# Kernel optimization log

Measured on AMD Instinct MI355X. Metric: run time of the kernel, lower is better.

Reference implementation:

```python
import jax, jax.numpy as jnp
import numpy as np

NEG_SLOPE = 0.2


def gat_conv(x, src, dst, W, a_src, a_dst, b, heads, out_ch, concat):
    """PyG-style GATConv (eval mode, self-loops already appended to src/dst)."""
    N = x.shape[0]
    h = (x @ W).reshape(N, heads, out_ch)            # [N,H,C]
    alpha_s = jnp.einsum('nhc,hc->nh', h, a_src)     # [N,H]
    alpha_d = jnp.einsum('nhc,hc->nh', h, a_dst)
    e = jax.nn.leaky_relu(alpha_s[src] + alpha_d[dst], NEG_SLOPE)  # [E,H]
    # segment softmax over incoming edges per destination node
    m = jax.ops.segment_max(e, dst, num_segments=N)  # every node has a self loop
    ex = jnp.exp(e - m[dst])
    denom = jax.ops.segment_sum(ex, dst, num_segments=N)
    alpha = ex / (denom[dst] + 1e-16)                # [E,H]
    msg = h[src] * alpha[:, :, None]                 # [E,H,C]
    out = jax.ops.segment_sum(msg, dst, num_segments=N)  # [N,H,C]
    if concat:
        out = out.reshape(N, heads * out_ch)
    else:
        out = out.mean(axis=1)
    return out + b


def setup_inputs() -> dict:
    key = jax.random.key(0)
    ks = jax.random.split(key, 12)
    N, E, F_IN = 100000, 3200000, 512
    H1, C1 = 8, 8           # conv1: heads=8, out=8, concat -> 64
    H2, C2 = 8, 16          # conv2: heads=8, out=num_classes=16, mean over heads
    x = jax.random.normal(ks[0], (N, F_IN), dtype=jnp.float32)
    edge_index = jax.random.randint(ks[1], (2, E), 0, N, dtype=jnp.int32)
    g = lambda k, s, fan: jax.random.normal(k, s, dtype=jnp.float32) / np.sqrt(fan)
    return {
        'x': x,
        'edge_index': edge_index,
        'W1': g(ks[2], (F_IN, H1 * C1), F_IN),
        'a_src1': g(ks[3], (H1, C1), C1),
        'a_dst1': g(ks[4], (H1, C1), C1),
        'b1': jnp.zeros((H1 * C1,), jnp.float32),
        'W2': g(ks[5], (H1 * C1, H2 * C2), H1 * C1),
        'a_src2': g(ks[6], (H2, C2), C2),
        'a_dst2': g(ks[7], (H2, C2), C2),
        'b2': jnp.zeros((C2,), jnp.float32),
    }


def reference(x, edge_index, W1, a_src1, a_dst1, b1, W2, a_src2, a_dst2, b2):
    N = x.shape[0]
    loops = jnp.arange(N, dtype=edge_index.dtype)
    src = jnp.concatenate([edge_index[0], loops])
    dst = jnp.concatenate([edge_index[1], loops])
    h = gat_conv(x, src, dst, W1, a_src1, a_dst1, b1, heads=8, out_ch=8, concat=True)
    h = jax.nn.elu(h)
    out = gat_conv(h, src, dst, W2, a_src2, a_dst2, b2, heads=8, out_ch=16, concat=False)
    return out
```

## Files before the change

kernel.cpp:

```cpp
#include <hip/hip_runtime.h>
#include <hip/hip_bf16.h>
#include <hip/hip_fp16.h>
#include <cstddef>

#define NEG_SLOPE 0.2f


__global__ __launch_bounds__(256) void bucket_hist_k(const int* __restrict__ dst, int E,
                                                     int* __restrict__ bhist, int NB) {
    __shared__ int lh[256];
    for (int t = threadIdx.x; t < 256; t += 256) lh[t] = 0;
    __syncthreads();
    int per = (E + gridDim.x - 1) / gridDim.x;
    int s = blockIdx.x * per;
    int e = min(s + per, E);
    for (int i = s + threadIdx.x; i < e; i += 256) atomicAdd(&lh[dst[i] >> 9], 1);
    __syncthreads();
    for (int t = threadIdx.x; t < NB; t += 256)
        if (lh[t]) atomicAdd(&bhist[t], lh[t]);
}

__global__ __launch_bounds__(256) void bucket_scan_k(const int* __restrict__ bhist, int NB,
                                                     int* __restrict__ bbase, int* __restrict__ cursor,
                                                     int* __restrict__ row_start, int N, int E) {
    __shared__ int tmp[256];
    int tid = threadIdx.x;
    int v = (tid < NB) ? bhist[tid] : 0;
    tmp[tid] = v;
    __syncthreads();
    for (int d = 1; d < 256; d <<= 1) {
        int t = tmp[tid];
        int a = (tid >= d) ? tmp[tid - d] : 0;
        __syncthreads();
        tmp[tid] = t + a;
        __syncthreads();
    }
    if (tid < NB) {
        int b = tmp[tid] - v;
        bbase[tid] = b;
        cursor[tid] = b;
    }
    if (tid == 0) {
        bbase[NB] = E;
        row_start[N] = E;
    }
}

__global__ __launch_bounds__(256) void partition_k(const int* __restrict__ src,
                                                   const int* __restrict__ dst, int E,
                                                   int* __restrict__ cursor,
                                                   unsigned int* __restrict__ part, int NB) {
    __shared__ int lh[256];
    __shared__ int lbase[256];
    for (int t = threadIdx.x; t < 256; t += 256) lh[t] = 0;
    __syncthreads();
    int per = (E + gridDim.x - 1) / gridDim.x;
    int s = blockIdx.x * per;
    int e = min(s + per, E);
    for (int i = s + threadIdx.x; i < e; i += 256) atomicAdd(&lh[dst[i] >> 9], 1);
    __syncthreads();
    for (int t = threadIdx.x; t < NB; t += 256) {
        int c = lh[t];
        lbase[t] = c ? atomicAdd(&cursor[t], c) : 0;
        lh[t] = 0;
    }
    __syncthreads();
    for (int i = s + threadIdx.x; i < e; i += 256) {
        int d = dst[i];
        int b = d >> 9;
        int lo = atomicAdd(&lh[b], 1);
        part[lbase[b] + lo] = ((unsigned)src[i] << 9) | (unsigned)(d & 511);
    }
}

__global__ __launch_bounds__(512) void bucket_build_k(const unsigned int* __restrict__ part,
                                                      const int* __restrict__ bbase,
                                                      int* __restrict__ row_start,
                                                      int* __restrict__ csr, int N) {
    __shared__ int cnt[512];
    __shared__ int cur[512];
    int b = blockIdx.x, tid = threadIdx.x;
    int n0 = b << 9;
    int s = bbase[b], e2 = bbase[b + 1];
    cnt[tid] = 0;
    __syncthreads();
    for (int i = s + tid; i < e2; i += 512) atomicAdd(&cnt[part[i] & 511], 1);
    __syncthreads();
    int v = cnt[tid];
    for (int d = 1; d < 512; d <<= 1) {
        int t = cnt[tid];
        int a = (tid >= d) ? cnt[tid - d] : 0;
        __syncthreads();
        cnt[tid] = t + a;
        __syncthreads();
    }
    int excl = cnt[tid] - v;
    if (n0 + tid < N) row_start[n0 + tid] = s + excl;
    cur[tid] = excl;
    __syncthreads();
    for (int i = s + tid; i < e2; i += 512) {
        unsigned u = part[i];
        int p = atomicAdd(&cur[u & 511], 1);
        csr[s + p] = (int)(u >> 9);
    }
}


#define BM 64
#define BN 64
#define BKT 32

__global__ __launch_bounds__(256) void sgemm_k(const float* __restrict__ A,
                                               const float* __restrict__ B,
                                               __half* __restrict__ C,
                                               int M, int Nc, int K) {
    __shared__ __align__(16) float As[BKT][BM + 4];
    __shared__ __align__(16) float Bs[BKT][BN];
    int bm = blockIdx.x * BM;
    int bn = blockIdx.y * BN;
    int t = threadIdx.x;
    int tc = t & 15;
    int tr = t >> 4;
    float acc[4][4] = {};

    for (int k0 = 0; k0 < K; k0 += BKT) {
        {
            int row = t >> 3;
            int kk = (t & 7) << 2;
#pragma unroll
            for (int p = 0; p < 2; ++p) {
                int r = row + p * 32;
                int gr = bm + r;
                float4 v = make_float4(0.f, 0.f, 0.f, 0.f);
                if (gr < M) v = *(const float4*)(A + (size_t)gr * K + k0 + kk);
                As[kk + 0][r] = v.x; As[kk + 1][r] = v.y;
                As[kk + 2][r] = v.z; As[kk + 3][r] = v.w;
            }
        }
        {
            int bk = t >> 4;
            int cc = (t & 15) << 2;
#pragma unroll
            for (int p = 0; p < 2; ++p) {
                int k = bk + p * 16;
                *(float4*)(&Bs[k][cc]) = *(const float4*)(B + (size_t)(k0 + k) * Nc + bn + cc);
            }
        }
        __syncthreads();
#pragma unroll
        for (int kk2 = 0; kk2 < BKT; ++kk2) {
            float4 a4 = *(const float4*)(&As[kk2][tr << 2]);
            float4 b4 = *(const float4*)(&Bs[kk2][tc << 2]);
            float av[4] = {a4.x, a4.y, a4.z, a4.w};
            float bv[4] = {b4.x, b4.y, b4.z, b4.w};
#pragma unroll
            for (int i = 0; i < 4; ++i)
#pragma unroll
                for (int j = 0; j < 4; ++j)
                    acc[i][j] = fmaf(av[i], bv[j], acc[i][j]);
        }
        __syncthreads();
    }
#pragma unroll
    for (int i = 0; i < 4; ++i) {
        int gr = bm + (tr << 2) + i;
        if (gr < M) {
            ushort4 p;
            p.x = __half_as_ushort(__float2half(acc[i][0]));
            p.y = __half_as_ushort(__float2half(acc[i][1]));
            p.z = __half_as_ushort(__float2half(acc[i][2]));
            p.w = __half_as_ushort(__float2half(acc[i][3]));
            *(ushort4*)(C + (size_t)gr * Nc + bn + (tc << 2)) = p;
        }
    }
}


template <int C>
__global__ void alpha_k(const __half* __restrict__ h, const float* __restrict__ a_s,
                        const float* __restrict__ a_d, float* __restrict__ os,
                        float* __restrict__ od, int NH) {
    int i = blockIdx.x * 256 + threadIdx.x;
    if (i >= NH) return;
    int hh = i & 7;
    const __half* hp = h + (size_t)i * C;
    float s = 0.f, d = 0.f;
#pragma unroll
    for (int c = 0; c < C; ++c) {
        float v = __half2float(hp[c]);
        s = fmaf(v, a_s[hh * C + c], s);
        d = fmaf(v, a_d[hh * C + c], d);
    }
    os[i] = s;
    od[i] = d;
}


__global__ __launch_bounds__(64) void aggregate1_k(
    const __half* __restrict__ h1, const float* __restrict__ as,
    const float* __restrict__ ad, const int* __restrict__ row_start,
    const int* __restrict__ csr, const float* __restrict__ b1,
    float* __restrict__ h1o, int N) {
    int n = blockIdx.x;
    int l = threadIdx.x;
    int h = l >> 3;
    int j = l & 7;
    int lbase = l & 56;
    float adv = ad[n * 8 + h];
    float e0 = as[n * 8 + h] + adv;
    e0 = fmaxf(e0, NEG_SLOPE * e0);
    float ex0 = __expf(e0);
    float denom = ex0;
    float acc = ex0 * __half2float(h1[(size_t)n * 64 + l]);
    int e = row_start[n], end = row_start[n + 1];
    int batched = e + ((end - e) & ~7);
    for (; e < batched; e += 8) {
        int sj = csr[e + j];
        float aj = as[sj * 8 + h];
        float t = aj + adv;
        t = fmaxf(t, NEG_SLOPE * t);
        float xj = __expf(t);
#pragma unroll
        for (int q = 0; q < 8; ++q) {
            int sq = __shfl(sj, q, 64);
            float xq = __shfl(xj, lbase + q, 64);
            float v = __half2float(h1[(size_t)sq * 64 + l]);
            denom += xq;
            acc = fmaf(xq, v, acc);
        }
    }
    for (; e < end; ++e) {
        int s0 = csr[e];
        float t = as[s0 * 8 + h] + adv;
        t = fmaxf(t, NEG_SLOPE * t);
        float x0 = __expf(t);
        denom += x0;
        acc = fmaf(x0, __half2float(h1[(size_t)s0 * 64 + l]), acc);
    }
    float v = acc / denom + b1[l];
    h1o[(size_t)n * 64 + l] = v > 0.f ? v : expm1f(v);
}


__global__ __launch_bounds__(64) void aggregate2_k(
    const __half* __restrict__ h2, const float* __restrict__ as,
    const float* __restrict__ ad, const int* __restrict__ row_start,
    const int* __restrict__ csr, const float* __restrict__ b2,
    float* __restrict__ out, int N) {
    int n = blockIdx.x;
    int l = threadIdx.x;
    int h = l >> 3;
    int j = l & 7;
    int lbase = l & 56;
    const __half2* H = (const __half2*)h2;
    float adv = ad[n * 8 + h];
    float e0 = as[n * 8 + h] + adv;
    e0 = fmaxf(e0, NEG_SLOPE * e0);
    float ex0 = __expf(e0);
    float denom = ex0;
    float2 self = __half22float2(H[(size_t)n * 64 + l]);
    float accx = ex0 * self.x, accy = ex0 * self.y;
    int e = row_start[n], end = row_start[n + 1];
    int batched = e + ((end - e) & ~7);
    for (; e < batched; e += 8) {
        int sj = csr[e + j];
        float aj = as[sj * 8 + h];
        float t = aj + adv;
        t = fmaxf(t, NEG_SLOPE * t);
        float xj = __expf(t);
#pragma unroll
        for (int q = 0; q < 8; ++q) {
            int sq = __shfl(sj, q, 64);
            float xq = __shfl(xj, lbase + q, 64);
            float2 v = __half22float2(H[(size_t)sq * 64 + l]);
            denom += xq;
            accx = fmaf(xq, v.x, accx);
            accy = fmaf(xq, v.y, accy);
        }
    }
    for (; e < end; ++e) {
        int s0 = csr[e];
        float t = as[s0 * 8 + h] + adv;
        t = fmaxf(t, NEG_SLOPE * t);
        float x0 = __expf(t);
        float2 v = __half22float2(H[(size_t)s0 * 64 + l]);
        denom += x0;
        accx = fmaf(x0, v.x, accx);
        accy = fmaf(x0, v.y, accy);
    }
    float rx = accx / denom, ry = accy / denom;
#pragma unroll
    for (int m = 8; m <= 32; m <<= 1) {
        rx += __shfl_xor(rx, m, 64);
        ry += __shfl_xor(ry, m, 64);
    }
    if (l < 8) {
        int c0 = l * 2;
        float2 o;
        o.x = rx * 0.125f + b2[c0];
        o.y = ry * 0.125f + b2[c0 + 1];
        *(float2*)(out + (size_t)n * 16 + c0) = o;
    }
}


extern "C" void kernel_launch(void* const* d_in, const int* in_sizes, int n_in,
                              void* d_out, int out_size, void* d_ws, size_t ws_size,
                              hipStream_t stream) {
    (void)n_in; (void)out_size; (void)ws_size;
    const float* x      = (const float*)d_in[0];
    const int*   ei     = (const int*)d_in[1];
    const float* W1     = (const float*)d_in[2];
    const float* a_src1 = (const float*)d_in[3];
    const float* a_dst1 = (const float*)d_in[4];
    const float* b1     = (const float*)d_in[5];
    const float* W2     = (const float*)d_in[6];
    const float* a_src2 = (const float*)d_in[7];
    const float* a_dst2 = (const float*)d_in[8];
    const float* b2     = (const float*)d_in[9];

    int N = in_sizes[0] / 512;
    int E = in_sizes[1] / 2;
    const int* src = ei;
    const int* dst = ei + E;
    int NB = (N + 511) >> 9;

    char* ws = (char*)d_ws;
    size_t off = 0;
    auto alloc = [&](size_t bytes) -> void* {
        void* p = ws + off;
        off = (off + bytes + 255) & ~(size_t)255;
        return p;
    };
    __half* h1  = (__half*)alloc((size_t)N * 64 * 2);
    float*  h1o = (float*)alloc((size_t)N * 64 * 4);
    __half* h2  = (__half*)alloc((size_t)N * 128 * 2);
    float* as1  = (float*)alloc((size_t)N * 8 * 4);
    float* ad1  = (float*)alloc((size_t)N * 8 * 4);
    float* as2  = (float*)alloc((size_t)N * 8 * 4);
    float* ad2  = (float*)alloc((size_t)N * 8 * 4);
    int* row_start = (int*)alloc((size_t)(N + 1) * 4);
    int* bhist     = (int*)alloc(256 * 4);
    int* bbase     = (int*)alloc(257 * 4);
    int* cursor    = (int*)alloc(256 * 4);
    unsigned int* part = (unsigned int*)alloc((size_t)E * 4);
    int* csr       = (int*)alloc((size_t)E * 4);

    hipMemsetAsync(bhist, 0, 256 * 4, stream);
    bucket_hist_k<<<512, 256, 0, stream>>>(dst, E, bhist, NB);
    bucket_scan_k<<<1, 256, 0, stream>>>(bhist, NB, bbase, cursor, row_start, N, E);
    partition_k<<<512, 256, 0, stream>>>(src, dst, E, cursor, part, NB);
    bucket_build_k<<<NB, 512, 0, stream>>>(part, bbase, row_start, csr, N);

    dim3 g1((N + BM - 1) / BM, 1);
    sgemm_k<<<g1, 256, 0, stream>>>(x, W1, h1, N, 64, 512);
    alpha_k<8><<<(N * 8 + 255) / 256, 256, 0, stream>>>(h1, a_src1, a_dst1, as1, ad1, N * 8);
    aggregate1_k<<<N, 64, 0, stream>>>(h1, as1, ad1, row_start, csr, b1, h1o, N);

    dim3 g2((N + BM - 1) / BM, 2);
    sgemm_k<<<g2, 256, 0, stream>>>(h1o, W2, h2, N, 128, 64);
    alpha_k<16><<<(N * 8 + 255) / 256, 256, 0, stream>>>(h2, a_src2, a_dst2, as2, ad2, N * 8);
    aggregate2_k<<<N, 64, 0, stream>>>(h2, as2, ad2, row_start, csr, b2, (float*)d_out, N);
}
```

Before: 714.8 us.

## Replace FP32 SIMT GEMMs with FP16 MFMA GEMMs and store h1o as half

Swaps the shared-memory FP32 SGEMM for a matrix-core kernel using 16x16x32 FP16 MFMA. The weights are converted to a transposed FP16 layout by a small kernel on every call, and the x activations are cast to FP16 on the fly. The first aggregate now writes its output in half precision, which halves the traffic into the second GEMM. The cost being targeted is FP32 ALU-bound GEMM time, mainly x@W1 with K=512. In exchange it loses precision on inputs and intermediates, and operands are loaded straight from global memory without LDS staging.

```diff
diff --git a/kernel.cpp b/kernel.cpp
--- a/kernel.cpp
+++ b/kernel.cpp
@@ -4,6 +4,9 @@
 #include <cstddef>
 
 #define NEG_SLOPE 0.2f
+
+typedef _Float16 half8 __attribute__((ext_vector_type(8)));
+typedef float floatx4 __attribute__((ext_vector_type(4)));
 
 
 __global__ __launch_bounds__(256) void bucket_hist_k(const int* __restrict__ dst, int E,
@@ -106,73 +109,53 @@
 }
 
 
-#define BM 64
-#define BN 64
-#define BKT 32
-
-__global__ __launch_bounds__(256) void sgemm_k(const float* __restrict__ A,
-                                               const float* __restrict__ B,
-                                               __half* __restrict__ C,
-                                               int M, int Nc, int K) {
-    __shared__ __align__(16) float As[BKT][BM + 4];
-    __shared__ __align__(16) float Bs[BKT][BN];
-    int bm = blockIdx.x * BM;
-    int bn = blockIdx.y * BN;
-    int t = threadIdx.x;
-    int tc = t & 15;
-    int tr = t >> 4;
-    float acc[4][4] = {};
-
-    for (int k0 = 0; k0 < K; k0 += BKT) {
-        {
-            int row = t >> 3;
-            int kk = (t & 7) << 2;
-#pragma unroll
-            for (int p = 0; p < 2; ++p) {
-                int r = row + p * 32;
-                int gr = bm + r;
-                float4 v = make_float4(0.f, 0.f, 0.f, 0.f);
-                if (gr < M) v = *(const float4*)(A + (size_t)gr * K + k0 + kk);
-                As[kk + 0][r] = v.x; As[kk + 1][r] = v.y;
-                As[kk + 2][r] = v.z; As[kk + 3][r] = v.w;
-            }
-        }
-        {
-            int bk = t >> 4;
-            int cc = (t & 15) << 2;
-#pragma unroll
-            for (int p = 0; p < 2; ++p) {
-                int k = bk + p * 16;
-                *(float4*)(&Bs[k][cc]) = *(const float4*)(B + (size_t)(k0 + k) * Nc + bn + cc);
-            }
-        }
-        __syncthreads();
-#pragma unroll
-        for (int kk2 = 0; kk2 < BKT; ++kk2) {
-            float4 a4 = *(const float4*)(&As[kk2][tr << 2]);
-            float4 b4 = *(const float4*)(&Bs[kk2][tc << 2]);
-            float av[4] = {a4.x, a4.y, a4.z, a4.w};
-            float bv[4] = {b4.x, b4.y, b4.z, b4.w};
-#pragma unroll
-            for (int i = 0; i < 4; ++i)
-#pragma unroll
-                for (int j = 0; j < 4; ++j)
-                    acc[i][j] = fmaf(av[i], bv[j], acc[i][j]);
-        }
-        __syncthreads();
-    }
-#pragma unroll
-    for (int i = 0; i < 4; ++i) {
-        int gr = bm + (tr << 2) + i;
-        if (gr < M) {
-            ushort4 p;
-            p.x = __half_as_ushort(__float2half(acc[i][0]));
-            p.y = __half_as_ushort(__float2half(acc[i][1]));
-            p.z = __half_as_ushort(__float2half(acc[i][2]));
-            p.w = __half_as_ushort(__float2half(acc[i][3]));
-            *(ushort4*)(C + (size_t)gr * Nc + bn + (tc << 2)) = p;
-        }
-    }
+__global__ void convw_k(const float* __restrict__ W, _Float16* __restrict__ WT,
+                        int K, int Nc) {
+    int i = blockIdx.x * 256 + threadIdx.x;
+    if (i < K * Nc) {
+        int k = i / Nc, n = i % Nc;
+        WT[(size_t)n * K + k] = (_Float16)W[i];
+    }
+}
+
+
+template <int NT, int K, bool AF32>
+__global__ __launch_bounds__(256) void mfma_gemm_k(const void* __restrict__ Av,
+                                                   const _Float16* __restrict__ BT,
+                                                   __half* __restrict__ C, int M) {
+    constexpr int Nc = NT * 16;
+    int wave = threadIdx.x >> 6, lane = threadIdx.x & 63;
+    int m16 = lane & 15, quad = lane >> 4;
+    int arow = blockIdx.x * 64 + wave * 16 + m16;
+    int arc = arow < M ? arow : M - 1;
+    floatx4 acc[NT] = {};
+    for (int k0 = 0; k0 < K; k0 += 32) {
+        half8 af;
+        if constexpr (AF32) {
+            const float* ap = (const float*)Av + (size_t)arc * K + k0 + quad * 8;
+            float4 v0 = *(const float4*)ap;
+            float4 v1 = *(const float4*)(ap + 4);
+            af[0] = (_Float16)v0.x; af[1] = (_Float16)v0.y;
+            af[2] = (_Float16)v0.z; af[3] = (_Float16)v0.w;
+            af[4] = (_Float16)v1.x; af[5] = (_Float16)v1.y;
+            af[6] = (_Float16)v1.z; af[7] = (_Float16)v1.w;
+        } else {
+            af = *(const half8*)((const _Float16*)Av + (size_t)arc * K + k0 + quad * 8);
+        }
+#pragma unroll
+        for (int t = 0; t < NT; ++t) {
+            half8 bf = *(const half8*)(BT + (size_t)(t * 16 + m16) * K + k0 + quad * 8);
+            acc[t] = __builtin_amdgcn_mfma_f32_16x16x32_f16(af, bf, acc[t], 0, 0, 0);
+        }
+    }
+    int gm0 = blockIdx.x * 64 + wave * 16 + quad * 4;
+#pragma unroll
+    for (int t = 0; t < NT; ++t)
+#pragma unroll
+        for (int r = 0; r < 4; ++r) {
+            int gm = gm0 + r;
+            if (gm < M) C[(size_t)gm * Nc + t * 16 + m16] = __float2half(acc[t][r]);
+        }
 }
 
 
@@ -200,7 +183,7 @@
     const __half* __restrict__ h1, const float* __restrict__ as,
     const float* __restrict__ ad, const int* __restrict__ row_start,
     const int* __restrict__ csr, const float* __restrict__ b1,
-    float* __restrict__ h1o, int N) {
+    __half* __restrict__ h1o, int N) {
     int n = blockIdx.x;
     int l = threadIdx.x;
     int h = l >> 3;
@@ -238,7 +221,7 @@
         acc = fmaf(x0, __half2float(h1[(size_t)s0 * 64 + l]), acc);
     }
     float v = acc / denom + b1[l];
-    h1o[(size_t)n * 64 + l] = v > 0.f ? v : expm1f(v);
+    h1o[(size_t)n * 64 + l] = __float2half(v > 0.f ? v : expm1f(v));
 }
 
 
@@ -333,12 +316,14 @@
         return p;
     };
     __half* h1  = (__half*)alloc((size_t)N * 64 * 2);
-    float*  h1o = (float*)alloc((size_t)N * 64 * 4);
+    __half* h1o = (__half*)alloc((size_t)N * 64 * 2);
     __half* h2  = (__half*)alloc((size_t)N * 128 * 2);
     float* as1  = (float*)alloc((size_t)N * 8 * 4);
     float* ad1  = (float*)alloc((size_t)N * 8 * 4);
     float* as2  = (float*)alloc((size_t)N * 8 * 4);
     float* ad2  = (float*)alloc((size_t)N * 8 * 4);
+    _Float16* W1T = (_Float16*)alloc((size_t)512 * 64 * 2);
+    _Float16* W2T = (_Float16*)alloc((size_t)64 * 128 * 2);
     int* row_start = (int*)alloc((size_t)(N + 1) * 4);
     int* bhist     = (int*)alloc(256 * 4);
     int* bbase     = (int*)alloc(257 * 4);
@@ -346,19 +331,22 @@
     unsigned int* part = (unsigned int*)alloc((size_t)E * 4);
     int* csr       = (int*)alloc((size_t)E * 4);
 
+    convw_k<<<(512 * 64 + 255) / 256, 256, 0, stream>>>(W1, W1T, 512, 64);
+    convw_k<<<(64 * 128 + 255) / 256, 256, 0, stream>>>(W2, W2T, 64, 128);
+
     hipMemsetAsync(bhist, 0, 256 * 4, stream);
     bucket_hist_k<<<512, 256, 0, stream>>>(dst, E, bhist, NB);
     bucket_scan_k<<<1, 256, 0, stream>>>(bhist, NB, bbase, cursor, row_start, N, E);
     partition_k<<<512, 256, 0, stream>>>(src, dst, E, cursor, part, NB);
     bucket_build_k<<<NB, 512, 0, stream>>>(part, bbase, row_start, csr, N);
 
-    dim3 g1((N + BM - 1) / BM, 1);
-    sgemm_k<<<g1, 256, 0, stream>>>(x, W1, h1, N, 64, 512);
+    int gblocks = (N + 63) / 64;
+
+    mfma_gemm_k<4, 512, true><<<gblocks, 256, 0, stream>>>(x, W1T, h1, N);
     alpha_k<8><<<(N * 8 + 255) / 256, 256, 0, stream>>>(h1, a_src1, a_dst1, as1, ad1, N * 8);
     aggregate1_k<<<N, 64, 0, stream>>>(h1, as1, ad1, row_start, csr, b1, h1o, N);
 
-    dim3 g2((N + BM - 1) / BM, 2);
-    sgemm_k<<<g2, 256, 0, stream>>>(h1o, W2, h2, N, 128, 64);
+    mfma_gemm_k<8, 64, false><<<gblocks, 256, 0, stream>>>(h1o, W2T, h2, N);
     alpha_k<16><<<(N * 8 + 255) / 256, 256, 0, stream>>>(h2, a_src2, a_dst2, as2, ad2, N * 8);
     aggregate2_k<<<N, 64, 0, stream>>>(h2, as2, ad2, row_start, csr, b2, (float*)d_out, N);
 }
```

After: 697.4 us. -2.4%, faster.
